# Performance work log

Hardware: AMD Instinct MI355X
Metric: run time of the kernel (lower is better)

## Reference

```python
import jax, jax.numpy as jnp
import numpy as np

HID = 100
NB_OUTPUT = 5


def _gru_layer(x, W_ih, W_hh, b_ih, b_hh):
    # x: [B, T, in] -> outputs [B, T, HID]; PyTorch GRU cell math, h0 = 0
    B = x.shape[0]
    H = W_hh.shape[1]

    def step(h, xt):
        gi = xt @ W_ih.T + b_ih            # [B, 3H]
        gh = h @ W_hh.T + b_hh             # [B, 3H]
        ir, iz, inn = jnp.split(gi, 3, axis=-1)
        hr, hz, hn = jnp.split(gh, 3, axis=-1)
        r = jax.nn.sigmoid(ir + hr)
        z = jax.nn.sigmoid(iz + hz)
        n = jnp.tanh(inn + r * hn)
        h_new = (1.0 - z) * n + z * h
        return h_new, h_new

    h0 = jnp.zeros((B, H), x.dtype)
    _, ys = jax.lax.scan(step, h0, jnp.swapaxes(x, 0, 1))  # ys: [T, B, H]
    return jnp.swapaxes(ys, 0, 1)


def setup_inputs() -> dict:
    key = jax.random.key(0)
    ks = jax.random.split(key, 12)
    B, T = 65536, 10
    s = 1.0 / np.sqrt(HID)
    u = lambda k, shape: jax.random.uniform(k, shape, jnp.float32, -s, s)
    return {
        "x": jax.random.normal(ks[0], (B, T), jnp.float32),
        # layer 0: input size 1
        "W_ih0": u(ks[1], (3 * HID, 1)),
        "W_hh0": u(ks[2], (3 * HID, HID)),
        "b_ih0": u(ks[3], (3 * HID,)),
        "b_hh0": u(ks[4], (3 * HID,)),
        # layer 1: input size HID
        "W_ih1": u(ks[5], (3 * HID, HID)),
        "W_hh1": u(ks[6], (3 * HID, HID)),
        "b_ih1": u(ks[7], (3 * HID,)),
        "b_hh1": u(ks[8], (3 * HID,)),
        # decode linear: HID -> 1
        "W_lin": u(ks[9], (1, HID)),
        "b_lin": u(ks[10], (1,)),
    }


def reference(x, W_ih0, W_hh0, b_ih0, b_hh0, W_ih1, W_hh1, b_ih1, b_hh1, W_lin, b_lin):
    B, T = x.shape
    vals = x[:, :, None]  # [B, T, 1]
    for _ in range(NB_OUTPUT):
        h1 = _gru_layer(vals, W_ih0, W_hh0, b_ih0, b_hh0)   # [B, T, HID]
        h2 = _gru_layer(h1, W_ih1, W_hh1, b_ih1, b_hh1)     # [B, T, HID]
        ret = h2[:, -1, :] @ W_lin.T + b_lin                # [B, 1]
        vals = jnp.concatenate([vals[:, 1:, :], ret[:, :, None]], axis=1)
    return vals[:, -NB_OUTPUT:, :]  # [B, 5, 1]
```

## Files before the change

### kernel.cpp

```cpp
#include <hip/hip_runtime.h>
#include <math.h>

#define HID 100
#define SEQT 10
#define NOUT 5
#define BTILE 64
#define NTHR 256
#define JPER 25
#define JC 5
#define NCHUNK 5

#define P0_FLOATS (20 * HID * 15)
#define P1_FLOATS (20 * HID * 30)

__device__ __forceinline__ float sigm(float x) {
    float e = __expf(-x);
    return __builtin_amdgcn_rcpf(1.0f + e);
}
__device__ __forceinline__ float tanh_fast(float x) {
    float e = __expf(-2.0f * x);
    return fmaf(2.0f, __builtin_amdgcn_rcpf(1.0f + e), -1.0f);
}

__global__ __launch_bounds__(256) void prep_kernel(
        const float* __restrict__ Whh0,
        const float* __restrict__ Wih1,
        const float* __restrict__ Whh1,
        float* __restrict__ ws) {
    int idx = blockIdx.x * blockDim.x + threadIdx.x;
    int stride = gridDim.x * blockDim.x;
    for (int i = idx; i < P0_FLOATS; i += stride) {
        int s = i % 15; int rest = i / 15;
        int k = rest % HID; int chunk = rest / HID;
        int g = s / JC, u = s % JC;
        ws[i] = Whh0[(g * HID + chunk * JC + u) * HID + k];
    }
    float* w1 = ws + P0_FLOATS;
    for (int i = idx; i < P1_FLOATS; i += stride) {
        int s = i % 30; int rest = i / 30;
        int k = rest % HID; int chunk = rest / HID;
        int m = s / 15;
        int g = (s % 15) / JC, u = s % JC;
        const float* src = m ? Whh1 : Wih1;
        w1[i] = src[(g * HID + chunk * JC + u) * HID + k];
    }
}

template <bool PACKED>
__global__ __launch_bounds__(NTHR, 2)
void gru_main(const float* __restrict__ x,
              const float* __restrict__ Wih0,
              const float* __restrict__ bih0, const float* __restrict__ bhh0,
              const float* __restrict__ bih1, const float* __restrict__ bhh1,
              const float* __restrict__ Wlin, const float* __restrict__ blin,
              const float* __restrict__ P0,
              const float* __restrict__ P1,
              const float* __restrict__ P1b,
              float* __restrict__ out) {
    __shared__ float h1s[HID][BTILE];
    __shared__ float h2s[HID][BTILE];
    __shared__ float seq[SEQT + NOUT][BTILE];

    const int tid = threadIdx.x;
    const int b = tid & (BTILE - 1);
    const int q = tid >> 6;
    const int chunkbase = __builtin_amdgcn_readfirstlane(q * NCHUNK);
    const int blockStart = blockIdx.x * BTILE;

    for (int i = tid; i < BTILE * SEQT; i += NTHR) {
        float v = x[blockStart * SEQT + i];
        int bb = i / SEQT;
        int tt = i - bb * SEQT;
        seq[tt][bb] = v;
    }
    __syncthreads();

    for (int it = 0; it < NOUT; ++it) {
        for (int i = tid; i < HID * BTILE; i += NTHR) {
            ((float*)h1s)[i] = 0.0f;
            ((float*)h2s)[i] = 0.0f;
        }
        __syncthreads();

        for (int t = 0; t < SEQT; ++t) {
            const float xt = seq[it + t][b];
            float hnew[JPER];

            #pragma unroll
            for (int c = 0; c < NCHUNK; ++c) {
                const int chunkid = chunkbase + c;
                const int j0 = chunkid * JC;
                float ar[JC], az[JC], ain[JC], ahn[JC];
                #pragma unroll
                for (int u = 0; u < JC; ++u) {
                    int j = j0 + u;
                    ar[u]  = fmaf(xt, Wih0[j],           bih0[j] + bhh0[j]);
                    az[u]  = fmaf(xt, Wih0[HID + j],     bih0[HID + j] + bhh0[HID + j]);
                    ain[u] = fmaf(xt, Wih0[2 * HID + j], bih0[2 * HID + j]);
                    ahn[u] = bhh0[2 * HID + j];
                }
                if (t > 0) {
                    for (int k = 0; k < HID; ++k) {
                        const float hk = h1s[k][b];
                        if constexpr (PACKED) {
                            const float* w = P0 + (chunkid * HID + k) * 15;
                            #pragma unroll
                            for (int u = 0; u < JC; ++u) {
                                ar[u]  = fmaf(hk, w[u],          ar[u]);
                                az[u]  = fmaf(hk, w[JC + u],     az[u]);
                                ahn[u] = fmaf(hk, w[2 * JC + u], ahn[u]);
                            }
                        } else {
                            #pragma unroll
                            for (int u = 0; u < JC; ++u) {
                                int j = j0 + u;
                                ar[u]  = fmaf(hk, P0[j * HID + k],             ar[u]);
                                az[u]  = fmaf(hk, P0[(HID + j) * HID + k],     az[u]);
                                ahn[u] = fmaf(hk, P0[(2 * HID + j) * HID + k], ahn[u]);
                            }
                        }
                    }
                }
                #pragma unroll
                for (int u = 0; u < JC; ++u) {
                    float r = sigm(ar[u]);
                    float z = sigm(az[u]);
                    float n = tanh_fast(fmaf(r, ahn[u], ain[u]));
                    float hold = (t > 0) ? h1s[j0 + u][b] : 0.0f;
                    hnew[c * JC + u] = fmaf(z, hold - n, n);
                }
            }
            __syncthreads();
            #pragma unroll
            for (int u = 0; u < JPER; ++u) h1s[chunkbase * JC + u][b] = hnew[u];
            __syncthreads();

            #pragma unroll
            for (int c = 0; c < NCHUNK; ++c) {
                const int chunkid = chunkbase + c;
                const int j0 = chunkid * JC;
                float ar[JC], az[JC], ain[JC], ahn[JC];
                #pragma unroll
                for (int u = 0; u < JC; ++u) {
                    int j = j0 + u;
                    ar[u]  = bih1[j] + bhh1[j];
                    az[u]  = bih1[HID + j] + bhh1[HID + j];
                    ain[u] = bih1[2 * HID + j];
                    ahn[u] = bhh1[2 * HID + j];
                }
                if (t > 0) {
                    for (int k = 0; k < HID; ++k) {
                        const float h1k = h1s[k][b];
                        const float h2k = h2s[k][b];
                        if constexpr (PACKED) {
                            const float* w = P1 + (chunkid * HID + k) * 30;
                            #pragma unroll
                            for (int u = 0; u < JC; ++u) {
                                ar[u]  = fmaf(h1k, w[u],          ar[u]);
                                az[u]  = fmaf(h1k, w[JC + u],     az[u]);
                                ain[u] = fmaf(h1k, w[2 * JC + u], ain[u]);
                                ar[u]  = fmaf(h2k, w[3 * JC + u], ar[u]);
                                az[u]  = fmaf(h2k, w[4 * JC + u], az[u]);
                                ahn[u] = fmaf(h2k, w[5 * JC + u], ahn[u]);
                            }
                        } else {
                            #pragma unroll
                            for (int u = 0; u < JC; ++u) {
                                int j = j0 + u;
                                ar[u]  = fmaf(h1k, P1[j * HID + k],              ar[u]);
                                az[u]  = fmaf(h1k, P1[(HID + j) * HID + k],      az[u]);
                                ain[u] = fmaf(h1k, P1[(2 * HID + j) * HID + k],  ain[u]);
                                ar[u]  = fmaf(h2k, P1b[j * HID + k],             ar[u]);
                                az[u]  = fmaf(h2k, P1b[(HID + j) * HID + k],     az[u]);
                                ahn[u] = fmaf(h2k, P1b[(2 * HID + j) * HID + k], ahn[u]);
                            }
                        }
                    }
                } else {
                    for (int k = 0; k < HID; ++k) {
                        const float h1k = h1s[k][b];
                        if constexpr (PACKED) {
                            const float* w = P1 + (chunkid * HID + k) * 30;
                            #pragma unroll
                            for (int u = 0; u < JC; ++u) {
                                ar[u]  = fmaf(h1k, w[u],          ar[u]);
                                az[u]  = fmaf(h1k, w[JC + u],     az[u]);
                                ain[u] = fmaf(h1k, w[2 * JC + u], ain[u]);
                            }
                        } else {
                            #pragma unroll
                            for (int u = 0; u < JC; ++u) {
                                int j = j0 + u;
                                ar[u]  = fmaf(h1k, P1[j * HID + k],             ar[u]);
                                az[u]  = fmaf(h1k, P1[(HID + j) * HID + k],     az[u]);
                                ain[u] = fmaf(h1k, P1[(2 * HID + j) * HID + k], ain[u]);
                            }
                        }
                    }
                }
                #pragma unroll
                for (int u = 0; u < JC; ++u) {
                    float r = sigm(ar[u]);
                    float z = sigm(az[u]);
                    float n = tanh_fast(fmaf(r, ahn[u], ain[u]));
                    float hold = (t > 0) ? h2s[j0 + u][b] : 0.0f;
                    hnew[c * JC + u] = fmaf(z, hold - n, n);
                }
            }
            __syncthreads();
            #pragma unroll
            for (int u = 0; u < JPER; ++u) h2s[chunkbase * JC + u][b] = hnew[u];
            __syncthreads();
        }

        if (q == 0) {
            float acc = blin[0];
            for (int k = 0; k < HID; ++k)
                acc = fmaf(h2s[k][b], Wlin[k], acc);
            out[(blockStart + b) * NOUT + it] = acc;
            seq[SEQT + it][b] = acc;
        }
        __syncthreads();
    }
}

extern "C" void kernel_launch(void* const* d_in, const int* in_sizes, int n_in,
                              void* d_out, int out_size, void* d_ws, size_t ws_size,
                              hipStream_t stream) {
    const float* x    = (const float*)d_in[0];
    const float* Wih0 = (const float*)d_in[1];
    const float* Whh0 = (const float*)d_in[2];
    const float* bih0 = (const float*)d_in[3];
    const float* bhh0 = (const float*)d_in[4];
    const float* Wih1 = (const float*)d_in[5];
    const float* Whh1 = (const float*)d_in[6];
    const float* bih1 = (const float*)d_in[7];
    const float* bhh1 = (const float*)d_in[8];
    const float* Wlin = (const float*)d_in[9];
    const float* blin = (const float*)d_in[10];
    float* out = (float*)d_out;

    const int B = in_sizes[0] / SEQT;
    const int nblocks = B / BTILE;

    const size_t packBytes = (size_t)(P0_FLOATS + P1_FLOATS) * sizeof(float);
    if (ws_size >= packBytes) {
        float* ws = (float*)d_ws;
        prep_kernel<<<90, 256, 0, stream>>>(Whh0, Wih1, Whh1, ws);
        gru_main<true><<<nblocks, NTHR, 0, stream>>>(
            x, Wih0, bih0, bhh0, bih1, bhh1, Wlin, blin,
            ws, ws + P0_FLOATS, nullptr, out);
    } else {
        gru_main<false><<<nblocks, NTHR, 0, stream>>>(
            x, Wih0, bih0, bhh0, bih1, bhh1, Wlin, blin,
            Whh0, Wih1, Whh1, out);
    }
}
```

Baseline: 15.41 ms.

## Raise occupancy to 3 blocks, precombine biases, keep inputs in registers

Launch bounds go from 2 to 3 blocks per SIMD/CU, and the shared sequence buffer becomes a small returns buffer, with the x inputs held in per-thread registers instead. The prep kernel now precomputes the combined GRU biases, so the main loop loads one array instead of adding two. The per-iteration zeroing of the h1s/h2s shared buffers is removed, which relies on t==0 never reading the old state. The tighter register budget from the higher occupancy target may cause spills in the unrolled FMA chains.

```diff
diff --git a/kernel.cpp b/kernel.cpp
--- a/kernel.cpp
+++ b/kernel.cpp
@@ -12,6 +12,7 @@
 
 #define P0_FLOATS (20 * HID * 15)
 #define P1_FLOATS (20 * HID * 30)
+#define CB_FLOATS (2 * 4 * HID)
 
 __device__ __forceinline__ float sigm(float x) {
     float e = __expf(-x);
@@ -26,6 +27,8 @@
         const float* __restrict__ Whh0,
         const float* __restrict__ Wih1,
         const float* __restrict__ Whh1,
+        const float* __restrict__ bih0, const float* __restrict__ bhh0,
+        const float* __restrict__ bih1, const float* __restrict__ bhh1,
         float* __restrict__ ws) {
     int idx = blockIdx.x * blockDim.x + threadIdx.x;
     int stride = gridDim.x * blockDim.x;
@@ -44,10 +47,24 @@
         const float* src = m ? Whh1 : Wih1;
         w1[i] = src[(g * HID + chunk * JC + u) * HID + k];
     }
+    float* cb = ws + P0_FLOATS + P1_FLOATS;
+    for (int i = idx; i < CB_FLOATS; i += stride) {
+        int which = i / (4 * HID);
+        int r = i % (4 * HID);
+        int g = r / HID; int j = r % HID;
+        const float* bi = which ? bih1 : bih0;
+        const float* bh = which ? bhh1 : bhh0;
+        float v;
+        if (g == 0)      v = bi[j] + bh[j];
+        else if (g == 1) v = bi[HID + j] + bh[HID + j];
+        else if (g == 2) v = bi[2 * HID + j];
+        else             v = bh[2 * HID + j];
+        cb[i] = v;
+    }
 }
 
 template <bool PACKED>
-__global__ __launch_bounds__(NTHR, 2)
+__global__ __launch_bounds__(NTHR, 3)
 void gru_main(const float* __restrict__ x,
               const float* __restrict__ Wih0,
               const float* __restrict__ bih0, const float* __restrict__ bhh0,
@@ -59,31 +76,39 @@
               float* __restrict__ out) {
     __shared__ float h1s[HID][BTILE];
     __shared__ float h2s[HID][BTILE];
-    __shared__ float seq[SEQT + NOUT][BTILE];
+    __shared__ float rets[NOUT][BTILE];
 
     const int tid = threadIdx.x;
     const int b = tid & (BTILE - 1);
     const int q = tid >> 6;
     const int chunkbase = __builtin_amdgcn_readfirstlane(q * NCHUNK);
+    const int jbase = chunkbase * JC;
     const int blockStart = blockIdx.x * BTILE;
 
-    for (int i = tid; i < BTILE * SEQT; i += NTHR) {
-        float v = x[blockStart * SEQT + i];
-        int bb = i / SEQT;
-        int tt = i - bb * SEQT;
-        seq[tt][bb] = v;
-    }
-    __syncthreads();
+    const float* CB0 = PACKED ? P1b : nullptr;
+    const float* CB1 = PACKED ? (P1b + 4 * HID) : nullptr;
+
+    float xr[SEQT];
+    {
+        const float* xp = x + (size_t)(blockStart + b) * SEQT;
+        #pragma unroll
+        for (int i = 0; i < SEQT; ++i) xr[i] = xp[i];
+    }
 
     for (int it = 0; it < NOUT; ++it) {
-        for (int i = tid; i < HID * BTILE; i += NTHR) {
-            ((float*)h1s)[i] = 0.0f;
-            ((float*)h2s)[i] = 0.0f;
-        }
-        __syncthreads();
-
         for (int t = 0; t < SEQT; ++t) {
-            const float xt = seq[it + t][b];
+            float xt;
+            {
+                const int s = it + t;
+                if (s < SEQT) {
+                    float v = xr[0];
+                    #pragma unroll
+                    for (int i = 1; i < SEQT; ++i) if (s == i) v = xr[i];
+                    xt = v;
+                } else {
+                    xt = rets[s - SEQT][b];
+                }
+            }
             float hnew[JPER];
 
             #pragma unroll
@@ -94,10 +119,17 @@
                 #pragma unroll
                 for (int u = 0; u < JC; ++u) {
                     int j = j0 + u;
-                    ar[u]  = fmaf(xt, Wih0[j],           bih0[j] + bhh0[j]);
-                    az[u]  = fmaf(xt, Wih0[HID + j],     bih0[HID + j] + bhh0[HID + j]);
-                    ain[u] = fmaf(xt, Wih0[2 * HID + j], bih0[2 * HID + j]);
-                    ahn[u] = bhh0[2 * HID + j];
+                    if constexpr (PACKED) {
+                        ar[u]  = fmaf(xt, Wih0[j],           CB0[j]);
+                        az[u]  = fmaf(xt, Wih0[HID + j],     CB0[HID + j]);
+                        ain[u] = fmaf(xt, Wih0[2 * HID + j], CB0[2 * HID + j]);
+                        ahn[u] = CB0[3 * HID + j];
+                    } else {
+                        ar[u]  = fmaf(xt, Wih0[j],           bih0[j] + bhh0[j]);
+                        az[u]  = fmaf(xt, Wih0[HID + j],     bih0[HID + j] + bhh0[HID + j]);
+                        ain[u] = fmaf(xt, Wih0[2 * HID + j], bih0[2 * HID + j]);
+                        ahn[u] = bhh0[2 * HID + j];
+                    }
                 }
                 if (t > 0) {
                     for (int k = 0; k < HID; ++k) {
@@ -132,7 +164,7 @@
             }
             __syncthreads();
             #pragma unroll
-            for (int u = 0; u < JPER; ++u) h1s[chunkbase * JC + u][b] = hnew[u];
+            for (int u = 0; u < JPER; ++u) h1s[jbase + u][b] = hnew[u];
             __syncthreads();
 
             #pragma unroll
@@ -143,10 +175,17 @@
                 #pragma unroll
                 for (int u = 0; u < JC; ++u) {
                     int j = j0 + u;
-                    ar[u]  = bih1[j] + bhh1[j];
-                    az[u]  = bih1[HID + j] + bhh1[HID + j];
-                    ain[u] = bih1[2 * HID + j];
-                    ahn[u] = bhh1[2 * HID + j];
+                    if constexpr (PACKED) {
+                        ar[u]  = CB1[j];
+                        az[u]  = CB1[HID + j];
+                        ain[u] = CB1[2 * HID + j];
+                        ahn[u] = CB1[3 * HID + j];
+                    } else {
+                        ar[u]  = bih1[j] + bhh1[j];
+                        az[u]  = bih1[HID + j] + bhh1[HID + j];
+                        ain[u] = bih1[2 * HID + j];
+                        ahn[u] = bhh1[2 * HID + j];
+                    }
                 }
                 if (t > 0) {
                     for (int k = 0; k < HID; ++k) {
@@ -209,7 +248,7 @@
             }
             __syncthreads();
             #pragma unroll
-            for (int u = 0; u < JPER; ++u) h2s[chunkbase * JC + u][b] = hnew[u];
+            for (int u = 0; u < JPER; ++u) h2s[jbase + u][b] = hnew[u];
             __syncthreads();
         }
 
@@ -218,7 +257,7 @@
             for (int k = 0; k < HID; ++k)
                 acc = fmaf(h2s[k][b], Wlin[k], acc);
             out[(blockStart + b) * NOUT + it] = acc;
-            seq[SEQT + it][b] = acc;
+            rets[it][b] = acc;
         }
         __syncthreads();
     }
@@ -243,13 +282,14 @@
     const int B = in_sizes[0] / SEQT;
     const int nblocks = B / BTILE;
 
-    const size_t packBytes = (size_t)(P0_FLOATS + P1_FLOATS) * sizeof(float);
+    const size_t packBytes = (size_t)(P0_FLOATS + P1_FLOATS + CB_FLOATS) * sizeof(float);
     if (ws_size >= packBytes) {
         float* ws = (float*)d_ws;
-        prep_kernel<<<90, 256, 0, stream>>>(Whh0, Wih1, Whh1, ws);
+        prep_kernel<<<90, 256, 0, stream>>>(Whh0, Wih1, Whh1,
+                                            bih0, bhh0, bih1, bhh1, ws);
         gru_main<true><<<nblocks, NTHR, 0, stream>>>(
             x, Wih0, bih0, bhh0, bih1, bhh1, Wlin, blin,
-            ws, ws + P0_FLOATS, nullptr, out);
+            ws, ws + P0_FLOATS, ws + P0_FLOATS + P1_FLOATS, out);
     } else {
         gru_main<false><<<nblocks, NTHR, 0, stream>>>(
             x, Wih0, bih0, bhh0, bih1, bhh1, Wlin, blin,
```

New measurement: 15.15 ms. No clear change (-1.7%).

## Pad packed GRU weights to float4 and software-pipeline vector weight loads

Applied to the files above, without the earlier changes.

Pads the packed recurrent weight layout to 16/32 floats per k so each step loads aligned float4 vectors. A v_mov zero offset forces the weight pointers into vector registers, so the loads become vector global loads rather than scalar ones. Loads are double-buffered in a manually unrolled k-loop. Biases and layer-0 input weights are prepacked into a per-chunk constant block. Inputs are kept in registers instead of a shared seq buffer, and the redundant per-iteration zeroing of hidden state is removed. The change raises register pressure and loads the uniform weights per lane, which costs extra VGPRs and more vector memory traffic.

```diff
diff --git a/kernel.cpp b/kernel.cpp
--- a/kernel.cpp
+++ b/kernel.cpp
@@ -10,8 +10,10 @@
 #define JC 5
 #define NCHUNK 5
 
-#define P0_FLOATS (20 * HID * 15)
-#define P1_FLOATS (20 * HID * 30)
+#define P0_FLOATS (20 * HID * 16)
+#define P1_FLOATS (20 * HID * 32)
+#define CBP_FLOATS (20 * 88)
+#define PACK_FLOATS (P0_FLOATS + P1_FLOATS + CBP_FLOATS)
 
 __device__ __forceinline__ float sigm(float x) {
     float e = __expf(-x);
@@ -23,43 +25,109 @@
 }
 
 __global__ __launch_bounds__(256) void prep_kernel(
+        const float* __restrict__ Wih0,
         const float* __restrict__ Whh0,
         const float* __restrict__ Wih1,
         const float* __restrict__ Whh1,
+        const float* __restrict__ bih0, const float* __restrict__ bhh0,
+        const float* __restrict__ bih1, const float* __restrict__ bhh1,
         float* __restrict__ ws) {
     int idx = blockIdx.x * blockDim.x + threadIdx.x;
     int stride = gridDim.x * blockDim.x;
     for (int i = idx; i < P0_FLOATS; i += stride) {
-        int s = i % 15; int rest = i / 15;
-        int k = rest % HID; int chunk = rest / HID;
-        int g = s / JC, u = s % JC;
-        ws[i] = Whh0[(g * HID + chunk * JC + u) * HID + k];
+        int s = i & 15; int rest = i >> 4;
+        int k = rest % HID; int c = rest / HID;
+        float v = 0.0f;
+        if (s < 15) { int g = s / JC, u = s % JC; v = Whh0[(g * HID + c * JC + u) * HID + k]; }
+        ws[i] = v;
     }
     float* w1 = ws + P0_FLOATS;
     for (int i = idx; i < P1_FLOATS; i += stride) {
-        int s = i % 30; int rest = i / 30;
-        int k = rest % HID; int chunk = rest / HID;
-        int m = s / 15;
-        int g = (s % 15) / JC, u = s % JC;
-        const float* src = m ? Whh1 : Wih1;
-        w1[i] = src[(g * HID + chunk * JC + u) * HID + k];
-    }
-}
-
-template <bool PACKED>
+        int s = i & 31; int rest = i >> 5;
+        int k = rest % HID; int c = rest / HID;
+        float v = 0.0f;
+        if (s < 15)                { int g = s / JC, u = s % JC;  v = Wih1[(g * HID + c * JC + u) * HID + k]; }
+        else if (s >= 16 && s < 31){ int s2 = s - 16; int g = s2 / JC, u = s2 % JC; v = Whh1[(g * HID + c * JC + u) * HID + k]; }
+        w1[i] = v;
+    }
+    float* cbp = ws + P0_FLOATS + P1_FLOATS;
+    for (int i = idx; i < CBP_FLOATS; i += stride) {
+        int c = i / 88; int r = i % 88;
+        int G = r / 8; int u = r % 8;
+        float v = 0.0f;
+        if (u < 5) {
+            int j = c * JC + u;
+            switch (G) {
+                case 0:  v = Wih0[j]; break;
+                case 1:  v = Wih0[HID + j]; break;
+                case 2:  v = Wih0[2 * HID + j]; break;
+                case 3:  v = bih0[j] + bhh0[j]; break;
+                case 4:  v = bih0[HID + j] + bhh0[HID + j]; break;
+                case 5:  v = bih0[2 * HID + j]; break;
+                case 6:  v = bhh0[2 * HID + j]; break;
+                case 7:  v = bih1[j] + bhh1[j]; break;
+                case 8:  v = bih1[HID + j] + bhh1[HID + j]; break;
+                case 9:  v = bih1[2 * HID + j]; break;
+                default: v = bhh1[2 * HID + j]; break;
+            }
+        }
+        cbp[i] = v;
+    }
+}
+
+#define LOADG(dst, base, G) { \
+    float4 _t4 = *(const float4*)((base) + (G) * 8); \
+    dst[0] = _t4.x; dst[1] = _t4.y; dst[2] = _t4.z; dst[3] = _t4.w; \
+    dst[4] = (base)[(G) * 8 + 4]; }
+
+#define LDW4(dst, idx) { \
+    dst[0] = wp[(idx) * 4 + 0]; dst[1] = wp[(idx) * 4 + 1]; \
+    dst[2] = wp[(idx) * 4 + 2]; dst[3] = wp[(idx) * 4 + 3]; }
+
+#define LDW8(dst, idx) { \
+    dst[0] = wp[(idx) * 8 + 0]; dst[1] = wp[(idx) * 8 + 1]; \
+    dst[2] = wp[(idx) * 8 + 2]; dst[3] = wp[(idx) * 8 + 3]; \
+    dst[4] = wp[(idx) * 8 + 4]; dst[5] = wp[(idx) * 8 + 5]; \
+    dst[6] = wp[(idx) * 8 + 6]; dst[7] = wp[(idx) * 8 + 7]; }
+
+#define LDW8IH(dst, idx) { \
+    dst[0] = wp[(idx) * 8 + 0]; dst[1] = wp[(idx) * 8 + 1]; \
+    dst[2] = wp[(idx) * 8 + 2]; dst[3] = wp[(idx) * 8 + 3]; }
+
+#define L0_STEP(W, hv) { \
+    ar[0]=fmaf(hv,W[0].x,ar[0]); ar[1]=fmaf(hv,W[0].y,ar[1]); ar[2]=fmaf(hv,W[0].z,ar[2]); ar[3]=fmaf(hv,W[0].w,ar[3]); ar[4]=fmaf(hv,W[1].x,ar[4]); \
+    az[0]=fmaf(hv,W[1].y,az[0]); az[1]=fmaf(hv,W[1].z,az[1]); az[2]=fmaf(hv,W[1].w,az[2]); az[3]=fmaf(hv,W[2].x,az[3]); az[4]=fmaf(hv,W[2].y,az[4]); \
+    ahn[0]=fmaf(hv,W[2].z,ahn[0]); ahn[1]=fmaf(hv,W[2].w,ahn[1]); ahn[2]=fmaf(hv,W[3].x,ahn[2]); ahn[3]=fmaf(hv,W[3].y,ahn[3]); ahn[4]=fmaf(hv,W[3].z,ahn[4]); }
+
+#define L1_IH(W, hv) { \
+    ar[0]=fmaf(hv,W[0].x,ar[0]); ar[1]=fmaf(hv,W[0].y,ar[1]); ar[2]=fmaf(hv,W[0].z,ar[2]); ar[3]=fmaf(hv,W[0].w,ar[3]); ar[4]=fmaf(hv,W[1].x,ar[4]); \
+    az[0]=fmaf(hv,W[1].y,az[0]); az[1]=fmaf(hv,W[1].z,az[1]); az[2]=fmaf(hv,W[1].w,az[2]); az[3]=fmaf(hv,W[2].x,az[3]); az[4]=fmaf(hv,W[2].y,az[4]); \
+    ain[0]=fmaf(hv,W[2].z,ain[0]); ain[1]=fmaf(hv,W[2].w,ain[1]); ain[2]=fmaf(hv,W[3].x,ain[2]); ain[3]=fmaf(hv,W[3].y,ain[3]); ain[4]=fmaf(hv,W[3].z,ain[4]); }
+
+#define L1_HH(W, hv) { \
+    ar[0]=fmaf(hv,W[4].x,ar[0]); ar[1]=fmaf(hv,W[4].y,ar[1]); ar[2]=fmaf(hv,W[4].z,ar[2]); ar[3]=fmaf(hv,W[4].w,ar[3]); ar[4]=fmaf(hv,W[5].x,ar[4]); \
+    az[0]=fmaf(hv,W[5].y,az[0]); az[1]=fmaf(hv,W[5].z,az[1]); az[2]=fmaf(hv,W[5].w,az[2]); az[3]=fmaf(hv,W[6].x,az[3]); az[4]=fmaf(hv,W[6].y,az[4]); \
+    ahn[0]=fmaf(hv,W[6].z,ahn[0]); ahn[1]=fmaf(hv,W[6].w,ahn[1]); ahn[2]=fmaf(hv,W[7].x,ahn[2]); ahn[3]=fmaf(hv,W[7].y,ahn[3]); ahn[4]=fmaf(hv,W[7].z,ahn[4]); }
+
+#define GATES(c, hsrc) { \
+    _Pragma("unroll") \
+    for (int u = 0; u < JC; ++u) { \
+        float r = sigm(ar[u]); \
+        float z = sigm(az[u]); \
+        float n = tanh_fast(fmaf(r, ahn[u], ain[u])); \
+        float hold = (t > 0) ? hsrc[j0 + u][b] : 0.0f; \
+        hnew[(c) * JC + u] = fmaf(z, hold - n, n); } }
+
 __global__ __launch_bounds__(NTHR, 2)
-void gru_main(const float* __restrict__ x,
-              const float* __restrict__ Wih0,
-              const float* __restrict__ bih0, const float* __restrict__ bhh0,
-              const float* __restrict__ bih1, const float* __restrict__ bhh1,
-              const float* __restrict__ Wlin, const float* __restrict__ blin,
-              const float* __restrict__ P0,
-              const float* __restrict__ P1,
-              const float* __restrict__ P1b,
-              float* __restrict__ out) {
+void gru_packed(const float* __restrict__ x,
+                const float* __restrict__ Wlin, const float* __restrict__ blin,
+                const float* __restrict__ P0,
+                const float* __restrict__ P1,
+                const float* __restrict__ CBP,
+                float* __restrict__ out) {
     __shared__ float h1s[HID][BTILE];
     __shared__ float h2s[HID][BTILE];
-    __shared__ float seq[SEQT + NOUT][BTILE];
+    __shared__ float rets[NOUT][BTILE];
 
     const int tid = threadIdx.x;
     const int b = tid & (BTILE - 1);
@@ -67,29 +135,174 @@
     const int chunkbase = __builtin_amdgcn_readfirstlane(q * NCHUNK);
     const int blockStart = blockIdx.x * BTILE;
 
-    for (int i = tid; i < BTILE * SEQT; i += NTHR) {
-        float v = x[blockStart * SEQT + i];
-        int bb = i / SEQT;
-        int tt = i - bb * SEQT;
-        seq[tt][bb] = v;
-    }
-    __syncthreads();
+    int dz; asm volatile("v_mov_b32 %0, 0" : "=v"(dz));
+    const float* P0v = P0 + dz;
+    const float* P1v = P1 + dz;
+    const float* CBv = CBP + dz;
+
+    float xr[SEQT];
+    {
+        const float* xp = x + (size_t)(blockStart + b) * SEQT;
+        #pragma unroll
+        for (int i = 0; i < SEQT; ++i) xr[i] = xp[i];
+    }
 
     for (int it = 0; it < NOUT; ++it) {
-        for (int i = tid; i < HID * BTILE; i += NTHR) {
-            ((float*)h1s)[i] = 0.0f;
-            ((float*)h2s)[i] = 0.0f;
-        }
-        __syncthreads();
-
         for (int t = 0; t < SEQT; ++t) {
-            const float xt = seq[it + t][b];
+            float xt;
+            {
+                const int s = it + t;
+                if (s < SEQT) {
+                    float v = xr[0];
+                    #pragma unroll
+                    for (int i = 1; i < SEQT; ++i) if (s == i) v = xr[i];
+                    xt = v;
+                } else {
+                    xt = rets[s - SEQT][b];
+                }
+            }
             float hnew[JPER];
 
             #pragma unroll
             for (int c = 0; c < NCHUNK; ++c) {
                 const int chunkid = chunkbase + c;
                 const int j0 = chunkid * JC;
+                const float* cb = CBv + chunkid * 88;
+                float wr[5], wz[5], wn[5], br[5], bz[5], bin[5], bhn[5];
+                LOADG(wr, cb, 0); LOADG(wz, cb, 1); LOADG(wn, cb, 2);
+                LOADG(br, cb, 3); LOADG(bz, cb, 4); LOADG(bin, cb, 5); LOADG(bhn, cb, 6);
+                float ar[JC], az[JC], ain[JC], ahn[JC];
+                #pragma unroll
+                for (int u = 0; u < JC; ++u) {
+                    ar[u]  = fmaf(xt, wr[u], br[u]);
+                    az[u]  = fmaf(xt, wz[u], bz[u]);
+                    ain[u] = fmaf(xt, wn[u], bin[u]);
+                    ahn[u] = bhn[u];
+                }
+                if (t > 0) {
+                    const float4* wp = (const float4*)P0v + (size_t)chunkid * HID * 4;
+                    float4 A[4], B[4], C[4], D[4];
+                    LDW4(A, 0); LDW4(B, 1);
+                    for (int k = 0; k < HID; k += 4) {
+                        LDW4(C, k + 2); LDW4(D, k + 3);
+                        float h0v = h1s[k][b], h1v = h1s[k + 1][b];
+                        L0_STEP(A, h0v); L0_STEP(B, h1v);
+                        LDW4(A, k + 4); LDW4(B, k + 5);
+                        float h2v = h1s[k + 2][b], h3v = h1s[k + 3][b];
+                        L0_STEP(C, h2v); L0_STEP(D, h3v);
+                    }
+                }
+                GATES(c, h1s);
+            }
+            __syncthreads();
+            #pragma unroll
+            for (int u = 0; u < JPER; ++u) h1s[chunkbase * JC + u][b] = hnew[u];
+            __syncthreads();
+
+            #pragma unroll
+            for (int c = 0; c < NCHUNK; ++c) {
+                const int chunkid = chunkbase + c;
+                const int j0 = chunkid * JC;
+                const float* cb = CBv + chunkid * 88;
+                float ar[JC], az[JC], ain[JC], ahn[JC];
+                {
+                    float br[5], bz[5], bin[5], bhn[5];
+                    LOADG(br, cb, 7); LOADG(bz, cb, 8); LOADG(bin, cb, 9); LOADG(bhn, cb, 10);
+                    #pragma unroll
+                    for (int u = 0; u < JC; ++u) { ar[u]=br[u]; az[u]=bz[u]; ain[u]=bin[u]; ahn[u]=bhn[u]; }
+                }
+                const float4* wp = (const float4*)P1v + (size_t)chunkid * HID * 8;
+                if (t > 0) {
+                    float4 A[8], B[8], C[8], D[8];
+                    LDW8(A, 0); LDW8(B, 1);
+                    for (int k = 0; k < HID; k += 4) {
+                        LDW8(C, k + 2); LDW8(D, k + 3);
+                        float g0 = h1s[k][b],     e0 = h2s[k][b];
+                        float g1 = h1s[k + 1][b], e1 = h2s[k + 1][b];
+                        L1_IH(A, g0); L1_HH(A, e0);
+                        L1_IH(B, g1); L1_HH(B, e1);
+                        LDW8(A, k + 4); LDW8(B, k + 5);
+                        float g2 = h1s[k + 2][b], e2 = h2s[k + 2][b];
+                        float g3 = h1s[k + 3][b], e3 = h2s[k + 3][b];
+                        L1_IH(C, g2); L1_HH(C, e2);
+                        L1_IH(D, g3); L1_HH(D, e3);
+                    }
+                } else {
+                    float4 A[4], B[4], C[4], D[4];
+                    LDW8IH(A, 0); LDW8IH(B, 1);
+                    for (int k = 0; k < HID; k += 4) {
+                        LDW8IH(C, k + 2); LDW8IH(D, k + 3);
+                        float g0 = h1s[k][b], g1 = h1s[k + 1][b];
+                        L1_IH(A, g0); L1_IH(B, g1);
+                        LDW8IH(A, k + 4); LDW8IH(B, k + 5);
+                        float g2 = h1s[k + 2][b], g3 = h1s[k + 3][b];
+                        L1_IH(C, g2); L1_IH(D, g3);
+                    }
+                }
+                GATES(c, h2s);
+            }
+            __syncthreads();
+            #pragma unroll
+            for (int u = 0; u < JPER; ++u) h2s[chunkbase * JC + u][b] = hnew[u];
+            __syncthreads();
+        }
+
+        if (q == 0) {
+            float acc = blin[0];
+            const float4* wl = (const float4*)Wlin;
+            #pragma unroll
+            for (int kk = 0; kk < HID / 4; ++kk) {
+                float4 wv = wl[kk];
+                acc = fmaf(h2s[4 * kk][b],     wv.x, acc);
+                acc = fmaf(h2s[4 * kk + 1][b], wv.y, acc);
+                acc = fmaf(h2s[4 * kk + 2][b], wv.z, acc);
+                acc = fmaf(h2s[4 * kk + 3][b], wv.w, acc);
+            }
+            out[(blockStart + b) * NOUT + it] = acc;
+            rets[it][b] = acc;
+        }
+        __syncthreads();
+    }
+}
+
+__global__ __launch_bounds__(NTHR, 2)
+void gru_fallback(const float* __restrict__ x,
+                  const float* __restrict__ Wih0, const float* __restrict__ Whh0,
+                  const float* __restrict__ bih0, const float* __restrict__ bhh0,
+                  const float* __restrict__ Wih1, const float* __restrict__ Whh1,
+                  const float* __restrict__ bih1, const float* __restrict__ bhh1,
+                  const float* __restrict__ Wlin, const float* __restrict__ blin,
+                  float* __restrict__ out) {
+    __shared__ float h1s[HID][BTILE];
+    __shared__ float h2s[HID][BTILE];
+    __shared__ float rets[NOUT][BTILE];
+    const int tid = threadIdx.x;
+    const int b = tid & (BTILE - 1);
+    const int q = tid >> 6;
+    const int chunkbase = __builtin_amdgcn_readfirstlane(q * NCHUNK);
+    const int blockStart = blockIdx.x * BTILE;
+    float xr[SEQT];
+    {
+        const float* xp = x + (size_t)(blockStart + b) * SEQT;
+        #pragma unroll
+        for (int i = 0; i < SEQT; ++i) xr[i] = xp[i];
+    }
+    for (int it = 0; it < NOUT; ++it) {
+        for (int t = 0; t < SEQT; ++t) {
+            float xt;
+            {
+                const int s = it + t;
+                if (s < SEQT) {
+                    float v = xr[0];
+                    #pragma unroll
+                    for (int i = 1; i < SEQT; ++i) if (s == i) v = xr[i];
+                    xt = v;
+                } else xt = rets[s - SEQT][b];
+            }
+            float hnew[JPER];
+            #pragma unroll
+            for (int c = 0; c < NCHUNK; ++c) {
+                const int j0 = (chunkbase + c) * JC;
                 float ar[JC], az[JC], ain[JC], ahn[JC];
                 #pragma unroll
                 for (int u = 0; u < JC; ++u) {
@@ -102,43 +315,24 @@
                 if (t > 0) {
                     for (int k = 0; k < HID; ++k) {
                         const float hk = h1s[k][b];
-                        if constexpr (PACKED) {
-                            const float* w = P0 + (chunkid * HID + k) * 15;
-                            #pragma unroll
-                            for (int u = 0; u < JC; ++u) {
-                                ar[u]  = fmaf(hk, w[u],          ar[u]);
-                                az[u]  = fmaf(hk, w[JC + u],     az[u]);
-                                ahn[u] = fmaf(hk, w[2 * JC + u], ahn[u]);
-                            }
-                        } else {
-                            #pragma unroll
-                            for (int u = 0; u < JC; ++u) {
-                                int j = j0 + u;
-                                ar[u]  = fmaf(hk, P0[j * HID + k],             ar[u]);
-                                az[u]  = fmaf(hk, P0[(HID + j) * HID + k],     az[u]);
-                                ahn[u] = fmaf(hk, P0[(2 * HID + j) * HID + k], ahn[u]);
-                            }
+                        #pragma unroll
+                        for (int u = 0; u < JC; ++u) {
+                            int j = j0 + u;
+                            ar[u]  = fmaf(hk, Whh0[j * HID + k],             ar[u]);
+                            az[u]  = fmaf(hk, Whh0[(HID + j) * HID + k],     az[u]);
+                            ahn[u] = fmaf(hk, Whh0[(2 * HID + j) * HID + k], ahn[u]);
                         }
                     }
                 }
-                #pragma unroll
-                for (int u = 0; u < JC; ++u) {
-                    float r = sigm(ar[u]);
-                    float z = sigm(az[u]);
-                    float n = tanh_fast(fmaf(r, ahn[u], ain[u]));
-                    float hold = (t > 0) ? h1s[j0 + u][b] : 0.0f;
-                    hnew[c * JC + u] = fmaf(z, hold - n, n);
-                }
+                GATES(c, h1s);
             }
             __syncthreads();
             #pragma unroll
             for (int u = 0; u < JPER; ++u) h1s[chunkbase * JC + u][b] = hnew[u];
             __syncthreads();
-
             #pragma unroll
             for (int c = 0; c < NCHUNK; ++c) {
-                const int chunkid = chunkbase + c;
-                const int j0 = chunkid * JC;
+                const int j0 = (chunkbase + c) * JC;
                 float ar[JC], az[JC], ain[JC], ahn[JC];
                 #pragma unroll
                 for (int u = 0; u < JC; ++u) {
@@ -148,77 +342,38 @@
                     ain[u] = bih1[2 * HID + j];
                     ahn[u] = bhh1[2 * HID + j];
                 }
-                if (t > 0) {
-                    for (int k = 0; k < HID; ++k) {
-                        const float h1k = h1s[k][b];
+                for (int k = 0; k < HID; ++k) {
+                    const float h1k = h1s[k][b];
+                    #pragma unroll
+                    for (int u = 0; u < JC; ++u) {
+                        int j = j0 + u;
+                        ar[u]  = fmaf(h1k, Wih1[j * HID + k],             ar[u]);
+                        az[u]  = fmaf(h1k, Wih1[(HID + j) * HID + k],     az[u]);
+                        ain[u] = fmaf(h1k, Wih1[(2 * HID + j) * HID + k], ain[u]);
+                    }
+                    if (t > 0) {
                         const float h2k = h2s[k][b];
-                        if constexpr (PACKED) {
-                            const float* w = P1 + (chunkid * HID + k) * 30;
-                            #pragma unroll
-                            for (int u = 0; u < JC; ++u) {
-                                ar[u]  = fmaf(h1k, w[u],          ar[u]);
-                                az[u]  = fmaf(h1k, w[JC + u],     az[u]);
-                                ain[u] = fmaf(h1k, w[2 * JC + u], ain[u]);
-                                ar[u]  = fmaf(h2k, w[3 * JC + u], ar[u]);
-                                az[u]  = fmaf(h2k, w[4 * JC + u], az[u]);
-                                ahn[u] = fmaf(h2k, w[5 * JC + u], ahn[u]);
-                            }
-                        } else {
-                            #pragma unroll
-                            for (int u = 0; u < JC; ++u) {
-                                int j = j0 + u;
-                                ar[u]  = fmaf(h1k, P1[j * HID + k],              ar[u]);
-                                az[u]  = fmaf(h1k, P1[(HID + j) * HID + k],      az[u]);
-                                ain[u] = fmaf(h1k, P1[(2 * HID + j) * HID + k],  ain[u]);
-                                ar[u]  = fmaf(h2k, P1b[j * HID + k],             ar[u]);
-                                az[u]  = fmaf(h2k, P1b[(HID + j) * HID + k],     az[u]);
-                                ahn[u] = fmaf(h2k, P1b[(2 * HID + j) * HID + k], ahn[u]);
-                            }
+                        #pragma unroll
+                        for (int u = 0; u < JC; ++u) {
+                            int j = j0 + u;
+                            ar[u]  = fmaf(h2k, Whh1[j * HID + k],             ar[u]);
+                            az[u]  = fmaf(h2k, Whh1[(HID + j) * HID + k],     az[u]);
+                            ahn[u] = fmaf(h2k, Whh1[(2 * HID + j) * HID + k], ahn[u]);
                         }
                     }
-                } else {
-                    for (int k = 0; k < HID; ++k) {
-                        const float h1k = h1s[k][b];
-                        if constexpr (PACKED) {
-                            const float* w = P1 + (chunkid * HID + k) * 30;
-                            #pragma unroll
-                            for (int u = 0; u < JC; ++u) {
-                                ar[u]  = fmaf(h1k, w[u],          ar[u]);
-                                az[u]  = fmaf(h1k, w[JC + u],     az[u]);
-                                ain[u] = fmaf(h1k, w[2 * JC + u], ain[u]);
-                            }
-                        } else {
-                            #pragma unroll
-                            for (int u = 0; u < JC; ++u) {
-                                int j = j0 + u;
-                                ar[u]  = fmaf(h1k, P1[j * HID + k],             ar[u]);
-                                az[u]  = fmaf(h1k, P1[(HID + j) * HID + k],     az[u]);
-                                ain[u] = fmaf(h1k, P1[(2 * HID + j) * HID + k], ain[u]);
-                            }
-                        }
-                    }
-                }
-                #pragma unroll
-                for (int u = 0; u < JC; ++u) {
-                    float r = sigm(ar[u]);
-                    float z = sigm(az[u]);
-                    float n = tanh_fast(fmaf(r, ahn[u], ain[u]));
-                    float hold = (t > 0) ? h2s[j0 + u][b] : 0.0f;
-                    hnew[c * JC + u] = fmaf(z, hold - n, n);
-                }
+                }
+                GATES(c, h2s);
             }
             __syncthreads();
             #pragma unroll
             for (int u = 0; u < JPER; ++u) h2s[chunkbase * JC + u][b] = hnew[u];
             __syncthreads();
         }
-
         if (q == 0) {
             float acc = blin[0];
-            for (int k = 0; k < HID; ++k)
-                acc = fmaf(h2s[k][b], Wlin[k], acc);
+            for (int k = 0; k < HID; ++k) acc = fmaf(h2s[k][b], Wlin[k], acc);
             out[(blockStart + b) * NOUT + it] = acc;
-            seq[SEQT + it][b] = acc;
+            rets[it][b] = acc;
         }
         __syncthreads();
     }
@@ -243,16 +398,15 @@
     const int B = in_sizes[0] / SEQT;
     const int nblocks = B / BTILE;
 
-    const size_t packBytes = (size_t)(P0_FLOATS + P1_FLOATS) * sizeof(float);
-    if (ws_size >= packBytes) {
+    if (ws_size >= (size_t)PACK_FLOATS * sizeof(float)) {
         float* ws = (float*)d_ws;
-        prep_kernel<<<90, 256, 0, stream>>>(Whh0, Wih1, Whh1, ws);
-        gru_main<true><<<nblocks, NTHR, 0, stream>>>(
-            x, Wih0, bih0, bhh0, bih1, bhh1, Wlin, blin,
-            ws, ws + P0_FLOATS, nullptr, out);
+        prep_kernel<<<90, 256, 0, stream>>>(Wih0, Whh0, Wih1, Whh1,
+                                            bih0, bhh0, bih1, bhh1, ws);
+        gru_packed<<<nblocks, NTHR, 0, stream>>>(
+            x, Wlin, blin,
+            ws, ws + P0_FLOATS, ws + P0_FLOATS + P1_FLOATS, out);
     } else {
-        gru_main<false><<<nblocks, NTHR, 0, stream>>>(
-            x, Wih0, bih0, bhh0, bih1, bhh1, Wlin, blin,
-            Whh0, Wih1, Whh1, out);
-    }
-}
+        gru_fallback<<<nblocks, NTHR, 0, stream>>>(
+            x, Wih0, Whh0, bih0, bhh0, Wih1, Whh1, bih1, bhh1, Wlin, blin, out);
+    }
+}
```

Result: slower. 33.18 ms (+115.3%).
